# Kernel tuning notes

Hardware: AMD Instinct MI355X
Metric: run time of the kernel (lower is better)

## Reference

```python
import jax, jax.numpy as jnp
import numpy as np

N = 65536   # instances (patches) in the bag
C = 512     # feature dim (mlp_dim)
P = 512     # number of prototypes (== C, required by the broadcast in the source)


def setup_inputs() -> dict:
    key = jax.random.key(0)
    k1, k2 = jax.random.split(key)
    x = jax.random.normal(k1, (1, N, C), dtype=jnp.float32)
    prototype = jax.random.normal(k2, (P, C), dtype=jnp.float32)
    return {"x": x, "prototype": prototype}


def reference(x, prototype):
    # x: (1, N, C) -> squeeze batch as in source
    xs = x[0]                                   # (N, C)
    # Euclidean cdist without materializing (P, N, C):
    # ||p - x||^2 = ||p||^2 + ||x||^2 - 2 p.x
    x_sq = jnp.sum(xs * xs, axis=1)             # (N,)
    p_sq = jnp.sum(prototype * prototype, axis=1)  # (P,)
    cross = jnp.einsum('pc,nc->pn', prototype, xs)  # (P, N)  -- the GEMM
    d2 = p_sq[:, None] + x_sq[None, :] - 2.0 * cross
    distances = jnp.sqrt(jnp.maximum(d2, 0.0))  # (P, N)
    # normalize by sqrt(C) (x.shape[1] after squeeze)
    distances = distances / jnp.sqrt(jnp.float32(C))
    inv_distances = 1.0 / distances             # (P, N)
    sum_inv = jnp.sum(inv_distances, axis=1, keepdims=True)  # (P, 1)
    weights = inv_distances / sum_inv           # (P, N)
    # weights.T: (N, P); elementwise with xs (N, C) -- valid since P == C
    x_out = weights.T * xs                      # (N, C)
    return (x_out, weights)
```

## Files before the change

### kernel.cpp

```cpp
#include <hip/hip_runtime.h>

typedef unsigned short ushort_t;
typedef __attribute__((ext_vector_type(8))) short bf16x8;
typedef __attribute__((ext_vector_type(4))) float f32x4;
typedef __attribute__((ext_vector_type(8))) unsigned short u16x8;

#define AS1 __attribute__((address_space(1)))
#define AS3 __attribute__((address_space(3)))

static __device__ __forceinline__ unsigned short f2bf(float f) {
    unsigned u = __float_as_uint(f);
    u += 0x7fffu + ((u >> 16) & 1u);
    return (unsigned short)(u >> 16);
}
static __device__ __forceinline__ float bf2f(unsigned short u) {
    return __uint_as_float(((unsigned)u) << 16);
}

__global__ __launch_bounds__(256) void prep_kernel(
    const float* __restrict__ src, ushort_t* __restrict__ dst,
    float* __restrict__ sq)
{
    const int row  = blockIdx.x * 4 + (threadIdx.x >> 6);
    const int lane = threadIdx.x & 63;
    const float4* s = (const float4*)(src + (size_t)row * 512);
    float4 v0 = s[lane * 2 + 0];
    float4 v1 = s[lane * 2 + 1];
    float ss = v0.x*v0.x + v0.y*v0.y + v0.z*v0.z + v0.w*v0.w
             + v1.x*v1.x + v1.y*v1.y + v1.z*v1.z + v1.w*v1.w;
    #pragma unroll
    for (int m = 32; m >= 1; m >>= 1) ss += __shfl_xor(ss, m);
    if (lane == 0) sq[row] = ss;
    u16x8 o;
    o[0]=f2bf(v0.x); o[1]=f2bf(v0.y); o[2]=f2bf(v0.z); o[3]=f2bf(v0.w);
    o[4]=f2bf(v1.x); o[5]=f2bf(v1.y); o[6]=f2bf(v1.z); o[7]=f2bf(v1.w);
    *(u16x8*)(dst + (size_t)row * 512 + lane * 8) = o;
}

template<int MODE>
__global__ __launch_bounds__(256, 4) void gemm_f32(
    const ushort_t* __restrict__ pb, const float* __restrict__ x,
    const float* __restrict__ p_sq, float* __restrict__ x_sq,
    const float* __restrict__ rcp, float* __restrict__ wout,
    float* __restrict__ xout, float* __restrict__ partial, int Nn)
{
    __shared__ __align__(16) char smem[33280];
    ushort_t* As = (ushort_t*)smem;
    ushort_t* Bs = (ushort_t*)(smem + 16384);

    const int tid  = threadIdx.x;
    const int lane = tid & 63, wid = tid >> 6;
    const int wm = wid >> 1, wn = wid & 1;
    const int l15 = lane & 15, l4 = lane >> 4;

    const int nwg = gridDim.x * gridDim.y;
    const int w   = blockIdx.x + gridDim.x * blockIdx.y;
    int orig = w;
    if ((nwg & 7) == 0) orig = (w & 7) * (nwg >> 3) + (w >> 3);
    const int m0 = (orig & 3) * 128;
    const int n0 = (orig >> 2) * 128;
    const int by = orig >> 2;

    f32x4 acc[4][4] = {};
    float ssq[4] = {0.f, 0.f, 0.f, 0.f};

    for (int kt = 0; kt < 512; kt += 64) {
        #pragma unroll
        for (int it = 0; it < 4; ++it) {
            const int cbase = it * 256 + wid * 64;
            const int cid   = cbase + lane;
            const int r     = cid >> 3;
            const int cl    = (cid & 7) ^ (r & 7);
            const ushort_t* ga = pb + (size_t)(m0 + r) * 512 + kt + cl * 8;
            __builtin_amdgcn_global_load_lds((const AS1 unsigned int*)ga,
                (AS3 unsigned int*)(As + cbase * 8), 16, 0, 0);
        }
        #pragma unroll
        for (int it = 0; it < 4; ++it) {
            const int g  = it * 256 + tid;
            const int r  = g >> 3;
            const int cl = g & 7;
            const float4* src = (const float4*)(x + (size_t)(n0 + r) * 512 + kt + cl * 8);
            const float4 f0 = src[0];
            const float4 f1 = src[1];
            if (MODE == 0)
                ssq[it] += f0.x*f0.x + f0.y*f0.y + f0.z*f0.z + f0.w*f0.w
                         + f1.x*f1.x + f1.y*f1.y + f1.z*f1.z + f1.w*f1.w;
            u16x8 o;
            o[0]=f2bf(f0.x); o[1]=f2bf(f0.y); o[2]=f2bf(f0.z); o[3]=f2bf(f0.w);
            o[4]=f2bf(f1.x); o[5]=f2bf(f1.y); o[6]=f2bf(f1.z); o[7]=f2bf(f1.w);
            *(u16x8*)&Bs[((size_t)(r * 8 + (cl ^ (r & 7)))) * 8] = o;
        }
        __syncthreads();
        #pragma unroll
        for (int kk = 0; kk < 2; ++kk) {
            bf16x8 a[4], b[4];
            #pragma unroll
            for (int mi = 0; mi < 4; ++mi) {
                const int rr = wm * 64 + mi * 16 + l15;
                const int c  = kk * 4 + l4;
                a[mi] = *(const bf16x8*)&As[(rr * 8 + (c ^ (rr & 7))) * 8];
            }
            #pragma unroll
            for (int ni = 0; ni < 4; ++ni) {
                const int rr = wn * 64 + ni * 16 + l15;
                const int c  = kk * 4 + l4;
                b[ni] = *(const bf16x8*)&Bs[(rr * 8 + (c ^ (rr & 7))) * 8];
            }
            #pragma unroll
            for (int mi = 0; mi < 4; ++mi)
                #pragma unroll
                for (int ni = 0; ni < 4; ++ni)
                    acc[mi][ni] = __builtin_amdgcn_mfma_f32_16x16x32_bf16(
                        a[mi], b[ni], acc[mi][ni], 0, 0, 0);
        }
        __syncthreads();
    }

    if (MODE == 0) {
        float* xsq_s = (float*)(smem + 16384);
        #pragma unroll
        for (int it = 0; it < 4; ++it) {
            float s = ssq[it];
            s += __shfl_xor(s, 1); s += __shfl_xor(s, 2); s += __shfl_xor(s, 4);
            if ((tid & 7) == 0) {
                const int r = it * 32 + (tid >> 3);
                xsq_s[r] = s;
                x_sq[n0 + r] = s;
            }
        }
        __syncthreads();

        float psum[4][4] = {};
        #pragma unroll
        for (int mi = 0; mi < 4; ++mi) {
            const int pbase = m0 + wm * 64 + mi * 16 + l4 * 4;
            const f32x4 ps4 = *(const f32x4*)(p_sq + pbase);
            #pragma unroll
            for (int ni = 0; ni < 4; ++ni) {
                const int nl = wn * 64 + ni * 16 + l15;
                const float xs = xsq_s[nl];
                #pragma unroll
                for (int j = 0; j < 4; ++j) {
                    float d2 = ps4[j] + xs - 2.0f * acc[mi][ni][j];
                    d2 = fmaxf(d2, 1e-20f);
                    psum[mi][j] += 22.62741699796952f * rsqrtf(d2);
                }
            }
        }
        #pragma unroll
        for (int mi = 0; mi < 4; ++mi)
            #pragma unroll
            for (int j = 0; j < 4; ++j) {
                float s = psum[mi][j];
                s += __shfl_xor(s, 1); s += __shfl_xor(s, 2);
                s += __shfl_xor(s, 4); s += __shfl_xor(s, 8);
                psum[mi][j] = s;
            }
        float* sp = (float*)smem;
        if (l15 == 0) {
            #pragma unroll
            for (int mi = 0; mi < 4; ++mi)
                #pragma unroll
                for (int j = 0; j < 4; ++j)
                    sp[(wm * 64 + mi * 16 + l4 * 4 + j) * 2 + wn] = psum[mi][j];
        }
        __syncthreads();
        if (tid < 128)
            partial[(size_t)(m0 + tid) * gridDim.y + by] =
                sp[tid * 2] + sp[tid * 2 + 1];
    } else {
        #pragma unroll
        for (int mi = 0; mi < 4; ++mi) {
            const int pbase = m0 + wm * 64 + mi * 16 + l4 * 4;
            const f32x4 ps4 = *(const f32x4*)(p_sq + pbase);
            const f32x4 rc4 = *(const f32x4*)(rcp + pbase);
            #pragma unroll
            for (int ni = 0; ni < 4; ++ni) {
                const int n = n0 + wn * 64 + ni * 16 + l15;
                const float xs = x_sq[n];
                #pragma unroll
                for (int j = 0; j < 4; ++j) {
                    float d2 = ps4[j] + xs - 2.0f * acc[mi][ni][j];
                    d2 = fmaxf(d2, 1e-20f);
                    const float w5 = 22.62741699796952f * rsqrtf(d2) * rc4[j];
                    acc[mi][ni][j] = w5;
                    wout[(size_t)(pbase + j) * Nn + n] = w5;
                }
            }
        }
        float (*Tr)[65] = (float(*)[65])smem;
        const int tx = tid & 15, ty = tid >> 4;
        #pragma unroll
        for (int h = 0; h < 2; ++h) {
            __syncthreads();
            if (wm == h) {
                #pragma unroll
                for (int mi = 0; mi < 4; ++mi)
                    #pragma unroll
                    for (int ni = 0; ni < 4; ++ni)
                        #pragma unroll
                        for (int j = 0; j < 4; ++j)
                            Tr[wn * 64 + ni * 16 + l15][mi * 16 + l4 * 4 + j]
                                = acc[mi][ni][j];
            }
            __syncthreads();
            #pragma unroll
            for (int rr = 0; rr < 8; ++rr) {
                const int nl = ty + rr * 16;
                const size_t gx = (size_t)(n0 + nl) * 512 + m0 + h * 64 + tx * 4;
                const float4 xv = *(const float4*)(x + gx);
                f32x4 ov;
                ov[0] = xv.x * Tr[nl][tx * 4 + 0];
                ov[1] = xv.y * Tr[nl][tx * 4 + 1];
                ov[2] = xv.z * Tr[nl][tx * 4 + 2];
                ov[3] = xv.w * Tr[nl][tx * 4 + 3];
                *(f32x4*)(xout + gx) = ov;
            }
        }
    }
}

__global__ __launch_bounds__(256) void rowsum_kernel(
    const float* __restrict__ partial, float* __restrict__ rcp, int nb)
{
    const int p = blockIdx.x;
    const int tid = threadIdx.x;
    float s = 0.0f;
    for (int i = tid; i < nb; i += 256) s += partial[(size_t)p * nb + i];
    #pragma unroll
    for (int m = 32; m >= 1; m >>= 1) s += __shfl_xor(s, m);
    __shared__ float red[4];
    if ((tid & 63) == 0) red[tid >> 6] = s;
    __syncthreads();
    if (tid == 0) rcp[p] = 1.0f / (red[0] + red[1] + red[2] + red[3]);
}

template<int MODE>
__global__ __launch_bounds__(256) void gemm_old(
    const ushort_t* __restrict__ pb, const ushort_t* __restrict__ xb,
    const float* __restrict__ p_sq, const float* __restrict__ x_sq,
    const float* __restrict__ rcp,
    float* __restrict__ wout, float* __restrict__ partial, int Nn)
{
    __shared__ __align__(16) char smem[33280];
    ushort_t* As = (ushort_t*)smem;
    ushort_t* Bs = (ushort_t*)(smem + 16384);
    const int tid  = threadIdx.x;
    const int lane = tid & 63, wid = tid >> 6;
    const int wm = wid >> 1, wn = wid & 1;
    const int l15 = lane & 15, l4 = lane >> 4;
    const int m0 = blockIdx.x * 128;
    const int n0 = blockIdx.y * 128;
    f32x4 acc[4][4] = {};
    for (int kt = 0; kt < 512; kt += 64) {
        #pragma unroll
        for (int it = 0; it < 4; ++it) {
            const int cbase = it * 256 + wid * 64;
            const int cid   = cbase + lane;
            const int r     = cid >> 3;
            const int cl    = (cid & 7) ^ (r & 7);
            const ushort_t* ga = pb + (size_t)(m0 + r) * 512 + kt + cl * 8;
            __builtin_amdgcn_global_load_lds((const AS1 unsigned int*)ga,
                (AS3 unsigned int*)(As + cbase * 8), 16, 0, 0);
            const ushort_t* gb = xb + (size_t)(n0 + r) * 512 + kt + cl * 8;
            __builtin_amdgcn_global_load_lds((const AS1 unsigned int*)gb,
                (AS3 unsigned int*)(Bs + cbase * 8), 16, 0, 0);
        }
        __syncthreads();
        #pragma unroll
        for (int kk = 0; kk < 2; ++kk) {
            bf16x8 a[4], b[4];
            #pragma unroll
            for (int mi = 0; mi < 4; ++mi) {
                const int rr = wm * 64 + mi * 16 + l15;
                const int c  = kk * 4 + l4;
                a[mi] = *(const bf16x8*)&As[(rr * 8 + (c ^ (rr & 7))) * 8];
            }
            #pragma unroll
            for (int ni = 0; ni < 4; ++ni) {
                const int rr = wn * 64 + ni * 16 + l15;
                const int c  = kk * 4 + l4;
                b[ni] = *(const bf16x8*)&Bs[(rr * 8 + (c ^ (rr & 7))) * 8];
            }
            #pragma unroll
            for (int mi = 0; mi < 4; ++mi)
                #pragma unroll
                for (int ni = 0; ni < 4; ++ni)
                    acc[mi][ni] = __builtin_amdgcn_mfma_f32_16x16x32_bf16(
                        a[mi], b[ni], acc[mi][ni], 0, 0, 0);
        }
        __syncthreads();
    }
    if (MODE == 0) {
        float psum[4][4] = {};
        #pragma unroll
        for (int mi = 0; mi < 4; ++mi) {
            const int pbase = m0 + wm * 64 + mi * 16 + l4 * 4;
            const f32x4 ps4 = *(const f32x4*)(p_sq + pbase);
            #pragma unroll
            for (int ni = 0; ni < 4; ++ni) {
                const int n = n0 + wn * 64 + ni * 16 + l15;
                const float xs = x_sq[n];
                #pragma unroll
                for (int j = 0; j < 4; ++j) {
                    float d2 = ps4[j] + xs - 2.0f * acc[mi][ni][j];
                    d2 = fmaxf(d2, 1e-20f);
                    psum[mi][j] += 22.62741699796952f * rsqrtf(d2);
                }
            }
        }
        #pragma unroll
        for (int mi = 0; mi < 4; ++mi)
            #pragma unroll
            for (int j = 0; j < 4; ++j) {
                float s = psum[mi][j];
                s += __shfl_xor(s, 1); s += __shfl_xor(s, 2);
                s += __shfl_xor(s, 4); s += __shfl_xor(s, 8);
                psum[mi][j] = s;
            }
        float* sp = (float*)smem;
        if (l15 == 0) {
            #pragma unroll
            for (int mi = 0; mi < 4; ++mi)
                #pragma unroll
                for (int j = 0; j < 4; ++j)
                    sp[(wm * 64 + mi * 16 + l4 * 4 + j) * 2 + wn] = psum[mi][j];
        }
        __syncthreads();
        if (tid < 128)
            partial[(size_t)(m0 + tid) * gridDim.y + blockIdx.y] =
                sp[tid * 2] + sp[tid * 2 + 1];
    } else {
        #pragma unroll
        for (int mi = 0; mi < 4; ++mi) {
            const int pbase = m0 + wm * 64 + mi * 16 + l4 * 4;
            const f32x4 ps4 = *(const f32x4*)(p_sq + pbase);
            const f32x4 rc4 = *(const f32x4*)(rcp + pbase);
            #pragma unroll
            for (int ni = 0; ni < 4; ++ni) {
                const int n = n0 + wn * 64 + ni * 16 + l15;
                const float xs = x_sq[n];
                #pragma unroll
                for (int j = 0; j < 4; ++j) {
                    float d2 = ps4[j] + xs - 2.0f * acc[mi][ni][j];
                    d2 = fmaxf(d2, 1e-20f);
                    wout[(size_t)(pbase + j) * Nn + n] =
                        22.62741699796952f * rsqrtf(d2) * rc4[j];
                }
            }
        }
    }
}

__global__ __launch_bounds__(256) void finalize2_kernel(
    const float* __restrict__ x, const float* __restrict__ w,
    float* __restrict__ xout, int Nn)
{
    __shared__ float T[64][65];
    const int tid = threadIdx.x;
    const int tx = tid & 15, ty = tid >> 4;
    const int p0 = blockIdx.x * 64, n0 = blockIdx.y * 64;
    #pragma unroll
    for (int rr = 0; rr < 4; ++rr) {
        const int pl = ty + rr * 16;
        const f32x4 wv = *(const f32x4*)(w + (size_t)(p0 + pl) * Nn + n0 + tx * 4);
        T[tx * 4 + 0][pl] = wv[0];
        T[tx * 4 + 1][pl] = wv[1];
        T[tx * 4 + 2][pl] = wv[2];
        T[tx * 4 + 3][pl] = wv[3];
    }
    __syncthreads();
    #pragma unroll
    for (int rr = 0; rr < 4; ++rr) {
        const int nl = ty + rr * 16;
        const size_t ix = (size_t)(n0 + nl) * 512 + p0 + tx * 4;
        const f32x4 xv = *(const f32x4*)(x + ix);
        f32x4 ov;
        ov[0] = xv[0] * T[nl][tx * 4 + 0];
        ov[1] = xv[1] * T[nl][tx * 4 + 1];
        ov[2] = xv[2] * T[nl][tx * 4 + 2];
        ov[3] = xv[3] * T[nl][tx * 4 + 3];
        *(f32x4*)(xout + ix) = ov;
    }
}

extern "C" void kernel_launch(void* const* d_in, const int* in_sizes, int n_in,
                              void* d_out, int out_size, void* d_ws, size_t ws_size,
                              hipStream_t stream)
{
    const float* x     = (const float*)d_in[0];
    const float* proto = (const float*)d_in[1];
    const int C = 512, P = 512;
    const int N = in_sizes[0] / C;
    const int NB = N / 128;

    float* xout = (float*)d_out;
    float* wout = xout + (size_t)N * C;

    const size_t pbf_b = (size_t)P * C * 2;
    const size_t need  = pbf_b + (size_t)P * 4 + (size_t)N * 4
                       + (size_t)P * NB * 4 + (size_t)P * 4;

    if (ws_size >= need) {
        char* scr = (char*)d_ws;
        ushort_t* pbf  = (ushort_t*)scr;
        float*    p_sq = (float*)(scr + pbf_b);
        float*    x_sq = p_sq + P;
        float*    part = x_sq + N;
        float*    rcp  = part + (size_t)P * NB;

        prep_kernel<<<P / 4, 256, 0, stream>>>(proto, pbf, p_sq);
        gemm_f32<0><<<dim3(P / 128, NB), 256, 0, stream>>>(
            pbf, x, p_sq, x_sq, nullptr, nullptr, nullptr, part, N);
        rowsum_kernel<<<P, 256, 0, stream>>>(part, rcp, NB);
        gemm_f32<1><<<dim3(P / 128, NB), 256, 0, stream>>>(
            pbf, x, p_sq, x_sq, rcp, wout, xout, nullptr, N);
    } else {
        char* scr = (char*)d_out;
        const size_t xb_b = (size_t)N * C * 2;
        ushort_t* xb   = (ushort_t*)scr;
        ushort_t* pbf  = (ushort_t*)(scr + xb_b);
        float*    x_sq = (float*)(scr + xb_b + pbf_b);
        float*    p_sq = x_sq + N;
        float*    part = p_sq + P;
        float*    rcp  = (float*)d_ws;

        prep_kernel<<<N / 4, 256, 0, stream>>>(x, xb, x_sq);
        prep_kernel<<<P / 4, 256, 0, stream>>>(proto, pbf, p_sq);
        gemm_old<0><<<dim3(P / 128, NB), 256, 0, stream>>>(
            pbf, xb, p_sq, x_sq, nullptr, nullptr, part, N);
        rowsum_kernel<<<P, 256, 0, stream>>>(part, rcp, NB);
        gemm_old<2><<<dim3(P / 128, NB), 256, 0, stream>>>(
            pbf, xb, p_sq, x_sq, rcp, wout, nullptr, N);
        finalize2_kernel<<<dim3(P / 64, N / 64), 256, 0, stream>>>(
            x, wout, xout, N);
    }
}
```

Baseline: 184.2 us.

## Store bf16 inverse distances once instead of recomputing GEMM in second pass

The second GEMM pass that recomputed distances is removed. The first pass now writes unnormalized inverse distances as bf16 into the output buffer as scratch, and a new streaming kernel scales them by the row reciprocal into the fp32 weights. A transpose kernel then forms x_out from x and the weights. This trades a full second GEMM over x for extra memory traffic (bf16 write and read, fp32 weight re-read in the transpose) and reduces weight precision to bf16 before normalization.

```diff
diff --git a/kernel.cpp b/kernel.cpp
--- a/kernel.cpp
+++ b/kernel.cpp
@@ -37,12 +37,10 @@
     *(u16x8*)(dst + (size_t)row * 512 + lane * 8) = o;
 }
 
-template<int MODE>
-__global__ __launch_bounds__(256, 4) void gemm_f32(
+__global__ __launch_bounds__(256, 4) void gemm_main(
     const ushort_t* __restrict__ pb, const float* __restrict__ x,
-    const float* __restrict__ p_sq, float* __restrict__ x_sq,
-    const float* __restrict__ rcp, float* __restrict__ wout,
-    float* __restrict__ xout, float* __restrict__ partial, int Nn)
+    const float* __restrict__ p_sq, ushort_t* __restrict__ inv_b,
+    float* __restrict__ partial, int Nn)
 {
     __shared__ __align__(16) char smem[33280];
     ushort_t* As = (ushort_t*)smem;
@@ -83,9 +81,8 @@
             const float4* src = (const float4*)(x + (size_t)(n0 + r) * 512 + kt + cl * 8);
             const float4 f0 = src[0];
             const float4 f1 = src[1];
-            if (MODE == 0)
-                ssq[it] += f0.x*f0.x + f0.y*f0.y + f0.z*f0.z + f0.w*f0.w
-                         + f1.x*f1.x + f1.y*f1.y + f1.z*f1.z + f1.w*f1.w;
+            ssq[it] += f0.x*f0.x + f0.y*f0.y + f0.z*f0.z + f0.w*f0.w
+                     + f1.x*f1.x + f1.y*f1.y + f1.z*f1.z + f1.w*f1.w;
             u16x8 o;
             o[0]=f2bf(f0.x); o[1]=f2bf(f0.y); o[2]=f2bf(f0.z); o[3]=f2bf(f0.w);
             o[4]=f2bf(f1.x); o[5]=f2bf(f1.y); o[6]=f2bf(f1.z); o[7]=f2bf(f1.w);
@@ -117,108 +114,56 @@
         __syncthreads();
     }
 
-    if (MODE == 0) {
-        float* xsq_s = (float*)(smem + 16384);
-        #pragma unroll
-        for (int it = 0; it < 4; ++it) {
-            float s = ssq[it];
-            s += __shfl_xor(s, 1); s += __shfl_xor(s, 2); s += __shfl_xor(s, 4);
-            if ((tid & 7) == 0) {
-                const int r = it * 32 + (tid >> 3);
-                xsq_s[r] = s;
-                x_sq[n0 + r] = s;
-            }
-        }
-        __syncthreads();
-
-        float psum[4][4] = {};
-        #pragma unroll
-        for (int mi = 0; mi < 4; ++mi) {
-            const int pbase = m0 + wm * 64 + mi * 16 + l4 * 4;
-            const f32x4 ps4 = *(const f32x4*)(p_sq + pbase);
-            #pragma unroll
-            for (int ni = 0; ni < 4; ++ni) {
-                const int nl = wn * 64 + ni * 16 + l15;
-                const float xs = xsq_s[nl];
-                #pragma unroll
-                for (int j = 0; j < 4; ++j) {
-                    float d2 = ps4[j] + xs - 2.0f * acc[mi][ni][j];
-                    d2 = fmaxf(d2, 1e-20f);
-                    psum[mi][j] += 22.62741699796952f * rsqrtf(d2);
-                }
-            }
-        }
+    float* xsq_s = (float*)(smem + 16384);
+    #pragma unroll
+    for (int it = 0; it < 4; ++it) {
+        float s = ssq[it];
+        s += __shfl_xor(s, 1); s += __shfl_xor(s, 2); s += __shfl_xor(s, 4);
+        if ((tid & 7) == 0) xsq_s[it * 32 + (tid >> 3)] = s;
+    }
+    __syncthreads();
+
+    float psum[4][4] = {};
+    #pragma unroll
+    for (int mi = 0; mi < 4; ++mi) {
+        const int pbase = m0 + wm * 64 + mi * 16 + l4 * 4;
+        const f32x4 ps4 = *(const f32x4*)(p_sq + pbase);
+        #pragma unroll
+        for (int ni = 0; ni < 4; ++ni) {
+            const int nl = wn * 64 + ni * 16 + l15;
+            const float xs = xsq_s[nl];
+            #pragma unroll
+            for (int j = 0; j < 4; ++j) {
+                float d2 = ps4[j] + xs - 2.0f * acc[mi][ni][j];
+                d2 = fmaxf(d2, 1e-20f);
+                const float iv = 22.62741699796952f * rsqrtf(d2);
+                acc[mi][ni][j] = iv;
+                psum[mi][j] += iv;
+                inv_b[(size_t)(pbase + j) * Nn + n0 + nl] = f2bf(iv);
+            }
+        }
+    }
+    #pragma unroll
+    for (int mi = 0; mi < 4; ++mi)
+        #pragma unroll
+        for (int j = 0; j < 4; ++j) {
+            float s = psum[mi][j];
+            s += __shfl_xor(s, 1); s += __shfl_xor(s, 2);
+            s += __shfl_xor(s, 4); s += __shfl_xor(s, 8);
+            psum[mi][j] = s;
+        }
+    float* sp = (float*)smem;
+    if (l15 == 0) {
         #pragma unroll
         for (int mi = 0; mi < 4; ++mi)
             #pragma unroll
-            for (int j = 0; j < 4; ++j) {
-                float s = psum[mi][j];
-                s += __shfl_xor(s, 1); s += __shfl_xor(s, 2);
-                s += __shfl_xor(s, 4); s += __shfl_xor(s, 8);
-                psum[mi][j] = s;
-            }
-        float* sp = (float*)smem;
-        if (l15 == 0) {
-            #pragma unroll
-            for (int mi = 0; mi < 4; ++mi)
-                #pragma unroll
-                for (int j = 0; j < 4; ++j)
-                    sp[(wm * 64 + mi * 16 + l4 * 4 + j) * 2 + wn] = psum[mi][j];
-        }
-        __syncthreads();
-        if (tid < 128)
-            partial[(size_t)(m0 + tid) * gridDim.y + by] =
-                sp[tid * 2] + sp[tid * 2 + 1];
-    } else {
-        #pragma unroll
-        for (int mi = 0; mi < 4; ++mi) {
-            const int pbase = m0 + wm * 64 + mi * 16 + l4 * 4;
-            const f32x4 ps4 = *(const f32x4*)(p_sq + pbase);
-            const f32x4 rc4 = *(const f32x4*)(rcp + pbase);
-            #pragma unroll
-            for (int ni = 0; ni < 4; ++ni) {
-                const int n = n0 + wn * 64 + ni * 16 + l15;
-                const float xs = x_sq[n];
-                #pragma unroll
-                for (int j = 0; j < 4; ++j) {
-                    float d2 = ps4[j] + xs - 2.0f * acc[mi][ni][j];
-                    d2 = fmaxf(d2, 1e-20f);
-                    const float w5 = 22.62741699796952f * rsqrtf(d2) * rc4[j];
-                    acc[mi][ni][j] = w5;
-                    wout[(size_t)(pbase + j) * Nn + n] = w5;
-                }
-            }
-        }
-        float (*Tr)[65] = (float(*)[65])smem;
-        const int tx = tid & 15, ty = tid >> 4;
-        #pragma unroll
-        for (int h = 0; h < 2; ++h) {
-            __syncthreads();
-            if (wm == h) {
-                #pragma unroll
-                for (int mi = 0; mi < 4; ++mi)
-                    #pragma unroll
-                    for (int ni = 0; ni < 4; ++ni)
-                        #pragma unroll
-                        for (int j = 0; j < 4; ++j)
-                            Tr[wn * 64 + ni * 16 + l15][mi * 16 + l4 * 4 + j]
-                                = acc[mi][ni][j];
-            }
-            __syncthreads();
-            #pragma unroll
-            for (int rr = 0; rr < 8; ++rr) {
-                const int nl = ty + rr * 16;
-                const size_t gx = (size_t)(n0 + nl) * 512 + m0 + h * 64 + tx * 4;
-                const float4 xv = *(const float4*)(x + gx);
-                f32x4 ov;
-                ov[0] = xv.x * Tr[nl][tx * 4 + 0];
-                ov[1] = xv.y * Tr[nl][tx * 4 + 1];
-                ov[2] = xv.z * Tr[nl][tx * 4 + 2];
-                ov[3] = xv.w * Tr[nl][tx * 4 + 3];
-                *(f32x4*)(xout + gx) = ov;
-            }
-        }
-    }
+            for (int j = 0; j < 4; ++j)
+                sp[(wm * 64 + mi * 16 + l4 * 4 + j) * 2 + wn] = psum[mi][j];
+    }
+    __syncthreads();
+    if (tid < 128)
+        partial[(size_t)(m0 + tid) * gridDim.y + by] =
+            sp[tid * 2] + sp[tid * 2 + 1];
 }
 
 __global__ __launch_bounds__(256) void rowsum_kernel(
@@ -234,6 +179,59 @@
     if ((tid & 63) == 0) red[tid >> 6] = s;
     __syncthreads();
     if (tid == 0) rcp[p] = 1.0f / (red[0] + red[1] + red[2] + red[3]);
+}
+
+__global__ __launch_bounds__(256) void finw_kernel(
+    const ushort_t* __restrict__ inv_b, const float* __restrict__ rcp,
+    float* __restrict__ w, int Nn)
+{
+    const int p = blockIdx.x >> 2;
+    const int q = blockIdx.x & 3;
+    const float rc = rcp[p];
+    const size_t base = (size_t)p * Nn + (size_t)q * (Nn >> 2);
+    const int chunks = (Nn >> 2) / 8;
+    for (int i = threadIdx.x; i < chunks; i += 256) {
+        const u16x8 v = *(const u16x8*)(inv_b + base + (size_t)i * 8);
+        f32x4 a, b;
+        a[0] = bf2f(v[0]) * rc; a[1] = bf2f(v[1]) * rc;
+        a[2] = bf2f(v[2]) * rc; a[3] = bf2f(v[3]) * rc;
+        b[0] = bf2f(v[4]) * rc; b[1] = bf2f(v[5]) * rc;
+        b[2] = bf2f(v[6]) * rc; b[3] = bf2f(v[7]) * rc;
+        *(f32x4*)(w + base + (size_t)i * 8)     = a;
+        *(f32x4*)(w + base + (size_t)i * 8 + 4) = b;
+    }
+}
+
+__global__ __launch_bounds__(256) void finalize2_kernel(
+    const float* __restrict__ x, const float* __restrict__ w,
+    float* __restrict__ xout, int Nn)
+{
+    __shared__ float T[64][65];
+    const int tid = threadIdx.x;
+    const int tx = tid & 15, ty = tid >> 4;
+    const int p0 = blockIdx.x * 64, n0 = blockIdx.y * 64;
+    #pragma unroll
+    for (int rr = 0; rr < 4; ++rr) {
+        const int pl = ty + rr * 16;
+        const f32x4 wv = *(const f32x4*)(w + (size_t)(p0 + pl) * Nn + n0 + tx * 4);
+        T[tx * 4 + 0][pl] = wv[0];
+        T[tx * 4 + 1][pl] = wv[1];
+        T[tx * 4 + 2][pl] = wv[2];
+        T[tx * 4 + 3][pl] = wv[3];
+    }
+    __syncthreads();
+    #pragma unroll
+    for (int rr = 0; rr < 4; ++rr) {
+        const int nl = ty + rr * 16;
+        const size_t ix = (size_t)(n0 + nl) * 512 + p0 + tx * 4;
+        const f32x4 xv = *(const f32x4*)(x + ix);
+        f32x4 ov;
+        ov[0] = xv[0] * T[nl][tx * 4 + 0];
+        ov[1] = xv[1] * T[nl][tx * 4 + 1];
+        ov[2] = xv[2] * T[nl][tx * 4 + 2];
+        ov[3] = xv[3] * T[nl][tx * 4 + 3];
+        *(f32x4*)(xout + ix) = ov;
+    }
 }
 
 template<int MODE>
@@ -353,38 +351,6 @@
     }
 }
 
-__global__ __launch_bounds__(256) void finalize2_kernel(
-    const float* __restrict__ x, const float* __restrict__ w,
-    float* __restrict__ xout, int Nn)
-{
-    __shared__ float T[64][65];
-    const int tid = threadIdx.x;
-    const int tx = tid & 15, ty = tid >> 4;
-    const int p0 = blockIdx.x * 64, n0 = blockIdx.y * 64;
-    #pragma unroll
-    for (int rr = 0; rr < 4; ++rr) {
-        const int pl = ty + rr * 16;
-        const f32x4 wv = *(const f32x4*)(w + (size_t)(p0 + pl) * Nn + n0 + tx * 4);
-        T[tx * 4 + 0][pl] = wv[0];
-        T[tx * 4 + 1][pl] = wv[1];
-        T[tx * 4 + 2][pl] = wv[2];
-        T[tx * 4 + 3][pl] = wv[3];
-    }
-    __syncthreads();
-    #pragma unroll
-    for (int rr = 0; rr < 4; ++rr) {
-        const int nl = ty + rr * 16;
-        const size_t ix = (size_t)(n0 + nl) * 512 + p0 + tx * 4;
-        const f32x4 xv = *(const f32x4*)(x + ix);
-        f32x4 ov;
-        ov[0] = xv[0] * T[nl][tx * 4 + 0];
-        ov[1] = xv[1] * T[nl][tx * 4 + 1];
-        ov[2] = xv[2] * T[nl][tx * 4 + 2];
-        ov[3] = xv[3] * T[nl][tx * 4 + 3];
-        *(f32x4*)(xout + ix) = ov;
-    }
-}
-
 extern "C" void kernel_launch(void* const* d_in, const int* in_sizes, int n_in,
                               void* d_out, int out_size, void* d_ws, size_t ws_size,
                               hipStream_t stream)
@@ -406,16 +372,17 @@
         char* scr = (char*)d_ws;
         ushort_t* pbf  = (ushort_t*)scr;
         float*    p_sq = (float*)(scr + pbf_b);
-        float*    x_sq = p_sq + P;
-        float*    part = x_sq + N;
+        float*    part = p_sq + P;
         float*    rcp  = part + (size_t)P * NB;
+        ushort_t* inv_b = (ushort_t*)d_out;
 
         prep_kernel<<<P / 4, 256, 0, stream>>>(proto, pbf, p_sq);
-        gemm_f32<0><<<dim3(P / 128, NB), 256, 0, stream>>>(
-            pbf, x, p_sq, x_sq, nullptr, nullptr, nullptr, part, N);
+        gemm_main<<<dim3(P / 128, NB), 256, 0, stream>>>(
+            pbf, x, p_sq, inv_b, part, N);
         rowsum_kernel<<<P, 256, 0, stream>>>(part, rcp, NB);
-        gemm_f32<1><<<dim3(P / 128, NB), 256, 0, stream>>>(
-            pbf, x, p_sq, x_sq, rcp, wout, xout, nullptr, N);
+        finw_kernel<<<P * 4, 256, 0, stream>>>(inv_b, rcp, wout, N);
+        finalize2_kernel<<<dim3(P / 64, N / 64), 256, 0, stream>>>(
+            x, wout, xout, N);
     } else {
         char* scr = (char*)d_out;
         const size_t xb_b = (size_t)N * C * 2;
```

Measured after the change: 216.1 us. 17.3% more time.
